# Kernel optimization log

Measured on AMD Instinct MI355X. Metric: run time of the kernel, lower is better.

The kernel has to match this reference:

```python
import jax, jax.numpy as jnp
import numpy as np
from jax import lax

B, C, H, W = 256, 3, 224, 224
M_MAG = 9.0  # RandAugment magnitude (init arg m)


def setup_inputs() -> dict:
    key = jax.random.key(0)
    k1, k2 = jax.random.split(key)
    # CIFAR-style normalization constants (as in the source module)
    mean = jnp.array([0.4914, 0.4822, 0.4465], dtype=jnp.float32)
    std = jnp.array([0.2023, 0.1994, 0.201], dtype=jnp.float32)
    # raw image in [0,1], then normalized (module expects normalized input)
    img = jax.random.uniform(k1, (B, C, H, W), dtype=jnp.float32)
    x = (img - mean[None, :, None, None]) / std[None, :, None, None]
    return {"x": x, "mean": mean, "std": std}


def _forward(x, mean, std):
    # deterministic op chain: sharpness -> contrast -> brightness -> solarize
    v_blend = M_MAG / 30.0 * (1.9 - 0.1) + 0.1   # 0.64 for sharpness/contrast/brightness
    v_sol = M_MAG / 30.0 * 1.0                    # 0.3 solarize threshold
    m_ = mean[None, :, None, None]
    s_ = std[None, :, None, None]

    # denormalize
    y = x * s_ + m_

    # sharpness: blend with 3x3 blur (kernel [[1,1,1],[1,5,1],[1,1,1]]/13, zero pad)
    k = jnp.array([[1., 1., 1.], [1., 5., 1.], [1., 1., 1.]], dtype=y.dtype) / 13.0
    kern = jnp.broadcast_to(k[None, None], (3, 1, 3, 3))  # depthwise OIHW
    blur = lax.conv_general_dilated(
        y, kern, window_strides=(1, 1), padding=[(1, 1), (1, 1)],
        feature_group_count=3, dimension_numbers=("NCHW", "OIHW", "NCHW"))
    y = y * v_blend + blur * (1.0 - v_blend)

    # contrast: blend with per-image mean of grayscale
    gray = 0.299 * y[:, 0] + 0.587 * y[:, 1] + 0.114 * y[:, 2]  # [B,H,W]
    gm = gray.mean(axis=(1, 2))[:, None, None, None]             # [B,1,1,1]
    y = y * v_blend + gm * (1.0 - v_blend)

    # brightness: blend with zeros
    y = y * v_blend

    # solarize: invert pixels >= threshold
    y = jnp.where(y < v_sol, y, 1.0 - y)

    # normalize
    return (y - m_) / s_


def reference(x, mean, std):
    return _forward(x, mean, std)
```

## Files before the change

### kernel.cpp

```cpp
#include <hip/hip_runtime.h>

#define IMG_B 256
#define IMG_H 224
#define IMG_W 224
#define HWPIX 50176
#define YP 228

#define FA(a,b) __fadd_rn((a),(b))
#define FM(a,b) __fmul_rn((a),(b))
#define FS(a,b) __fsub_rn((a),(b))
#define FD(a,b) __fdiv_rn((a),(b))

typedef float nt4 __attribute__((ext_vector_type(4)));

__device__ __forceinline__ float VBF()   { return (float)(9.0/30.0*(1.9-0.1)+0.1); }
__device__ __forceinline__ float OMVBF() { return (float)(1.0 - (9.0/30.0*(1.9-0.1)+0.1)); }
__device__ __forceinline__ float VSF()   { return (float)(9.0/30.0*1.0); }

__device__ __forceinline__ void y1_from_rows(const float* yU, const float* yC,
                                             const float* yD, float* y1o) {
    const float WN = 1.0f / 13.0f, WC = 5.0f / 13.0f;
#pragma unroll
    for (int mm = 0; mm < 4; ++mm) {
        float acc = 0.0f;
        acc = FA(acc, FM(WN, yU[mm + 0]));
        acc = FA(acc, FM(WN, yU[mm + 1]));
        acc = FA(acc, FM(WN, yU[mm + 2]));
        acc = FA(acc, FM(WN, yC[mm + 0]));
        acc = FA(acc, FM(WC, yC[mm + 1]));
        acc = FA(acc, FM(WN, yC[mm + 2]));
        acc = FA(acc, FM(WN, yD[mm + 0]));
        acc = FA(acc, FM(WN, yD[mm + 1]));
        acc = FA(acc, FM(WN, yD[mm + 2]));
        y1o[mm] = FA(FM(yC[mm + 1], VBF()), FM(acc, OMVBF()));
    }
}

__device__ __forceinline__ void stage_load(const float* __restrict__ xc, int r0,
                                           int t, float4* pf) {
#pragma unroll
    for (int u = 0; u < 4; ++u) {
        const int idx = t + 256 * u;
        float4 v = make_float4(0.f, 0.f, 0.f, 0.f);
        if (idx < 896) {
            const int row = idx / 56, c4 = (idx % 56) * 4;
            const int gi = r0 - 1 + row;
            if (gi >= 0 && gi < IMG_H)
                v = *(const float4*)(xc + (size_t)gi * IMG_W + c4);
        }
        pf[u] = v;
    }
}

__device__ __forceinline__ void stage_write(float s, float m, int r0, int t,
                                            const float4* pf, float* __restrict__ Y,
                                            int P) {
#pragma unroll
    for (int u = 0; u < 4; ++u) {
        const int idx = t + 256 * u;
        if (idx < 896) {
            const int row = idx / 56, c4 = (idx % 56) * 4;
            const int gi = r0 - 1 + row;
            float4 w;
            if (gi >= 0 && gi < IMG_H) {
                w.x = FA(FM(pf[u].x, s), m);
                w.y = FA(FM(pf[u].y, s), m);
                w.z = FA(FM(pf[u].z, s), m);
                w.w = FA(FM(pf[u].w, s), m);
            } else {
                w.x = w.y = w.z = w.w = 0.0f;
            }
            *(float4*)(&Y[row * P + c4]) = w;
        }
    }
}

__device__ __forceinline__ void lds_y6(const float* __restrict__ r, int j, float* y6) {
    const float4 vC = *(const float4*)(r + j);
    const float4 vL = *(const float4*)(r + (j > 0 ? j - 4 : 0));
    const float4 vR = *(const float4*)(r + (j + 4 < IMG_W ? j + 4 : IMG_W - 4));
    y6[0] = (j > 0) ? vL.w : 0.0f;
    y6[1] = vC.x; y6[2] = vC.y; y6[3] = vC.z; y6[4] = vC.w;
    y6[5] = (j + 4 < IMG_W) ? vR.x : 0.0f;
}

__global__ __launch_bounds__(256, 4) void kA1(const float* __restrict__ x,
                                              const float* __restrict__ mean_,
                                              const float* __restrict__ std_,
                                              float* __restrict__ part) {
    const int swz = (blockIdx.x & 7) * 512 + (blockIdx.x >> 3);
    const int ck = swz & 15, b = swz >> 4;
    const int t = threadIdx.x;
    const int r0 = ck * 14;

    __shared__ float SM[3648];
    float* Y  = SM;
    float* G2 = SM;
    float* CH = SM + 3328;
    float* LS = SM + 3584;

    const int rg  = t / 56;
    const int col = t - rg * 56;
    const bool active = (t < 224);
    const int rcount = (rg < 2) ? 4 : 3;
    const int rstart = (rg < 2) ? rg * 4 : 8 + (rg - 2) * 3;
    const int jd = col * 4;
    const bool lwave = ((t & 63) == 0)  && (col > 0);
    const bool rwave = ((t & 63) == 63) && (col < 55);

    const float s0 = std_[0], s1 = std_[1], s2 = std_[2];
    const float m0 = mean_[0], m1 = mean_[1], m2 = mean_[2];
    const float C0 = 0.299f, C1 = 0.587f, C2 = 0.114f;

    float4 q0[4], q1[4], q2[4];
#pragma unroll
    for (int u = 0; u < 4; ++u) {
        const int idx = t + 256 * u;
        q0[u] = q1[u] = q2[u] = make_float4(0.f, 0.f, 0.f, 0.f);
        if (idx < 896) {
            const int row = idx / 56, c4 = (idx % 56) * 4;
            const int gi = r0 - 1 + row;
            if (gi >= 0 && gi < IMG_H) {
                const float* p = x + (size_t)b * 3 * HWPIX + (size_t)gi * IMG_W + c4;
                q0[u] = *(const float4*)(p);
                q1[u] = *(const float4*)(p + HWPIX);
                q2[u] = *(const float4*)(p + 2 * HWPIX);
            }
        }
    }
#define GRAY1(a0v, a1v, a2v)                                              \
    FA(FA(FM(C0, FA(FM(a0v, s0), m0)), FM(C1, FA(FM(a1v, s1), m1))),      \
       FM(C2, FA(FM(a2v, s2), m2)))
#pragma unroll
    for (int u = 0; u < 4; ++u) {
        const int idx = t + 256 * u;
        if (idx < 896) {
            const int row = idx / 56, c4 = (idx % 56) * 4;
            const int gi = r0 - 1 + row;
            float4 w = make_float4(0.f, 0.f, 0.f, 0.f);
            if (gi >= 0 && gi < IMG_H) {
                w.x = GRAY1(q0[u].x, q1[u].x, q2[u].x);
                w.y = GRAY1(q0[u].y, q1[u].y, q2[u].y);
                w.z = GRAY1(q0[u].z, q1[u].z, q2[u].z);
                w.w = GRAY1(q0[u].w, q1[u].w, q2[u].w);
            }
            *(float4*)(&Y[row * YP + c4]) = w;
        }
    }
#undef GRAY1
    __syncthreads();

#define LOADROW(V, LWv, RWv, yr) do {                                 \
        V   = *(const float4*)(&Y[(yr) * YP + jd]);                   \
        LWv = __shfl_up(V.w, 1, 64);                                  \
        RWv = __shfl_down(V.x, 1, 64);                                \
        if (lwave) LWv = Y[(yr) * YP + jd - 1];                       \
        if (rwave) RWv = Y[(yr) * YP + jd + 4];                       \
    } while (0)

#define FILL6(y6, V, LWv, RWv) do {                                   \
        y6[0] = (col > 0) ? LWv : 0.0f;                               \
        y6[1] = V.x; y6[2] = V.y; y6[3] = V.z; y6[4] = V.w;           \
        y6[5] = (col < 55) ? RWv : 0.0f;                              \
    } while (0)

    float4 gacc[4];

    if (active) {
        float4 v0, v1, v2;
        float la0, la1, la2, ra0, ra1, ra2;
        LOADROW(v0, la0, ra0, rstart);
        LOADROW(v1, la1, ra1, rstart + 1);
#pragma unroll
        for (int k = 0; k < 4; ++k) {
            if (k < rcount) {
                LOADROW(v2, la2, ra2, rstart + k + 2);
                float yU[6], yC[6], yD[6], y1g[4];
                FILL6(yU, v0, la0, ra0);
                FILL6(yC, v1, la1, ra1);
                FILL6(yD, v2, la2, ra2);
                y1_from_rows(yU, yC, yD, y1g);
                gacc[k].x = y1g[0]; gacc[k].y = y1g[1];
                gacc[k].z = y1g[2]; gacc[k].w = y1g[3];
                v0 = v1; la0 = la1; ra0 = ra1;
                v1 = v2; la1 = la2; ra1 = ra2;
            }
        }
    }
    __syncthreads();

    if (active) {
#pragma unroll
        for (int k = 0; k < 4; ++k) {
            if (k < rcount) {
                const int pl = (rstart + k) * IMG_W + jd;
                const int grp = pl / 392;
                const int rem = pl - grp * 392;
                int li = rem / 96; if (li > 3) li = 3;
                const int o = rem - 96 * li;
                *(float4*)(&G2[(grp * 4 + li) * 104 + o]) = gacc[k];
            }
        }
    }
    __syncthreads();

    {
        const int leaf = t >> 3, e = t & 7;
        const int base = leaf * 104 + e;
        const int nk = ((leaf & 3) == 3) ? 13 : 12;
        float r = G2[base];
        for (int k = 1; k < nk; ++k) r = FA(r, G2[base + 8 * k]);
        CH[t] = r;
    }
    __syncthreads();

    if (t < 32) {
        const float* c8 = &CH[t * 8];
        LS[t] = FA(FA(FA(c8[0], c8[1]), FA(c8[2], c8[3])),
                   FA(FA(c8[4], c8[5]), FA(c8[6], c8[7])));
    }
    __syncthreads();

    if (t == 0) {
        float v[32];
#pragma unroll
        for (int k = 0; k < 32; ++k) v[k] = LS[k];
        for (int n = 16; n >= 1; n >>= 1)
            for (int k = 0; k < n; ++k) v[k] = FA(v[2 * k], v[2 * k + 1]);
        part[swz] = v[0];
    }
#undef LOADROW
#undef FILL6
}

__global__ __launch_bounds__(256) void kB(const float* __restrict__ x,
                                          const float* __restrict__ mean_,
                                          const float* __restrict__ std_,
                                          const float* __restrict__ part,
                                          float* __restrict__ out) {
    const int swz = ((int)blockIdx.x & 7) * 1536 + ((int)blockIdx.x >> 3);
    const int ck = swz & 15;
    const int r1 = swz >> 4;
    const int c  = r1 % 3;
    const int b  = r1 / 3;
    const int t  = threadIdx.x;
    const int r0 = ck * 14;

    __shared__ float Y[16 * IMG_W];
    __shared__ float gsh;

    const float s = std_[c], m = mean_[c];
    float4 pf[4];
    stage_load(x + (size_t)(b * 3 + c) * HWPIX, r0, t, pf);

    if (t == 0) {
        float v[16];
#pragma unroll
        for (int k = 0; k < 16; ++k) v[k] = part[b * 16 + k];
#pragma unroll
        for (int n = 8; n >= 1; n >>= 1)
#pragma unroll
            for (int k = 0; k < 8; ++k)
                if (k < n) v[k] = FA(v[2 * k], v[2 * k + 1]);
        gsh = FD(v[0], 50176.0f);
    }

    stage_write(s, m, r0, t, pf, Y, IMG_W);
    __syncthreads();
    const float g = gsh;

    float* oc = out + (size_t)(b * 3 + c) * HWPIX + (size_t)r0 * IMG_W;

    for (int qi = t; qi < 784; qi += 256) {
        const int lr = qi / 56 + 1, j = (qi % 56) * 4;
        float yU[6], yC[6], yD[6], y1[4];
        lds_y6(&Y[(lr - 1) * IMG_W], j, yU);
        lds_y6(&Y[lr * IMG_W],       j, yC);
        lds_y6(&Y[(lr + 1) * IMG_W], j, yD);
        y1_from_rows(yU, yC, yD, y1);

        nt4 o4;
#pragma unroll
        for (int mm = 0; mm < 4; ++mm) {
            const float y2 = FA(FM(y1[mm], VBF()), FM(g, OMVBF()));
            const float y3 = FM(y2, VBF());
            const float y4 = (y3 < VSF()) ? y3 : FS(1.0f, y3);
            o4[mm] = FD(FS(y4, m), s);
        }
        __builtin_nontemporal_store(o4, (nt4*)(oc + (size_t)(lr - 1) * IMG_W + j));
    }
}

extern "C" void kernel_launch(void* const* d_in, const int* in_sizes, int n_in,
                              void* d_out, int out_size, void* d_ws, size_t ws_size,
                              hipStream_t stream) {
    const float* x     = (const float*)d_in[0];
    const float* mean_ = (const float*)d_in[1];
    const float* std_  = (const float*)d_in[2];
    float* out = (float*)d_out;

    float* part = (float*)d_ws;

    kA1<<<IMG_B * 16, 256, 0, stream>>>(x, mean_, std_, part);

    kB<<<IMG_B * 3 * 16, 256, 0, stream>>>(x, mean_, std_, part, out);
}
```

Before: 77.04 us.

## Load raw tile directly to LDS and denormalize on read; shuffle-reduce partials

kB now copies the raw input halo tile from global memory straight into LDS with global_load_lds, instead of staging through registers and writing denormalized values. The denormalize affine is applied when values are read back from LDS, and out-of-range halo rows are clamped on load and zeroed on read. This removes the register round-trip and the separate LDS write pass, at the cost of redoing the multiply-add on each of the repeated stencil reads. In kA1, the last 32-way reduction is done with wave shuffles, which drops one LDS buffer, one barrier and the serial single-thread sum.

```diff
diff --git a/kernel.cpp b/kernel.cpp
--- a/kernel.cpp
+++ b/kernel.cpp
@@ -1,4 +1,5 @@
 #include <hip/hip_runtime.h>
+#include <stdint.h>
 
 #define IMG_B 256
 #define IMG_H 224
@@ -36,52 +37,22 @@
     }
 }
 
-__device__ __forceinline__ void stage_load(const float* __restrict__ xc, int r0,
-                                           int t, float4* pf) {
-#pragma unroll
-    for (int u = 0; u < 4; ++u) {
-        const int idx = t + 256 * u;
-        float4 v = make_float4(0.f, 0.f, 0.f, 0.f);
-        if (idx < 896) {
-            const int row = idx / 56, c4 = (idx % 56) * 4;
-            const int gi = r0 - 1 + row;
-            if (gi >= 0 && gi < IMG_H)
-                v = *(const float4*)(xc + (size_t)gi * IMG_W + c4);
-        }
-        pf[u] = v;
-    }
-}
-
-__device__ __forceinline__ void stage_write(float s, float m, int r0, int t,
-                                            const float4* pf, float* __restrict__ Y,
-                                            int P) {
-#pragma unroll
-    for (int u = 0; u < 4; ++u) {
-        const int idx = t + 256 * u;
-        if (idx < 896) {
-            const int row = idx / 56, c4 = (idx % 56) * 4;
-            const int gi = r0 - 1 + row;
-            float4 w;
-            if (gi >= 0 && gi < IMG_H) {
-                w.x = FA(FM(pf[u].x, s), m);
-                w.y = FA(FM(pf[u].y, s), m);
-                w.z = FA(FM(pf[u].z, s), m);
-                w.w = FA(FM(pf[u].w, s), m);
-            } else {
-                w.x = w.y = w.z = w.w = 0.0f;
-            }
-            *(float4*)(&Y[row * P + c4]) = w;
-        }
-    }
-}
-
-__device__ __forceinline__ void lds_y6(const float* __restrict__ r, int j, float* y6) {
+__device__ __forceinline__ void ldsx_y6(const float* __restrict__ r, int j,
+                                        bool rowvalid, float s, float m, float* y6) {
+    if (!rowvalid) {
+#pragma unroll
+        for (int q = 0; q < 6; ++q) y6[q] = 0.0f;
+        return;
+    }
     const float4 vC = *(const float4*)(r + j);
     const float4 vL = *(const float4*)(r + (j > 0 ? j - 4 : 0));
     const float4 vR = *(const float4*)(r + (j + 4 < IMG_W ? j + 4 : IMG_W - 4));
-    y6[0] = (j > 0) ? vL.w : 0.0f;
-    y6[1] = vC.x; y6[2] = vC.y; y6[3] = vC.z; y6[4] = vC.w;
-    y6[5] = (j + 4 < IMG_W) ? vR.x : 0.0f;
+    y6[0] = (j > 0) ? FA(FM(vL.w, s), m) : 0.0f;
+    y6[1] = FA(FM(vC.x, s), m);
+    y6[2] = FA(FM(vC.y, s), m);
+    y6[3] = FA(FM(vC.z, s), m);
+    y6[4] = FA(FM(vC.w, s), m);
+    y6[5] = (j + 4 < IMG_W) ? FA(FM(vR.x, s), m) : 0.0f;
 }
 
 __global__ __launch_bounds__(256, 4) void kA1(const float* __restrict__ x,
@@ -97,7 +68,6 @@
     float* Y  = SM;
     float* G2 = SM;
     float* CH = SM + 3328;
-    float* LS = SM + 3584;
 
     const int rg  = t / 56;
     const int col = t - rg * 56;
@@ -216,18 +186,15 @@
 
     if (t < 32) {
         const float* c8 = &CH[t * 8];
-        LS[t] = FA(FA(FA(c8[0], c8[1]), FA(c8[2], c8[3])),
-                   FA(FA(c8[4], c8[5]), FA(c8[6], c8[7])));
-    }
-    __syncthreads();
-
-    if (t == 0) {
-        float v[32];
-#pragma unroll
-        for (int k = 0; k < 32; ++k) v[k] = LS[k];
-        for (int n = 16; n >= 1; n >>= 1)
-            for (int k = 0; k < n; ++k) v[k] = FA(v[2 * k], v[2 * k + 1]);
-        part[swz] = v[0];
+        float vv = FA(FA(FA(c8[0], c8[1]), FA(c8[2], c8[3])),
+                      FA(FA(c8[4], c8[5]), FA(c8[6], c8[7])));
+#pragma unroll
+        for (int n = 16; n >= 1; n >>= 1) {
+            const float lo = __shfl(vv, 2 * t, 64);
+            const float hi = __shfl(vv, 2 * t + 1, 64);
+            vv = FA(lo, hi);
+        }
+        if (t == 0) part[swz] = vv;
     }
 #undef LOADROW
 #undef FILL6
@@ -246,12 +213,25 @@
     const int t  = threadIdx.x;
     const int r0 = ck * 14;
 
-    __shared__ float Y[16 * IMG_W];
+    __shared__ float X[16 * IMG_W];
     __shared__ float gsh;
 
     const float s = std_[c], m = mean_[c];
-    float4 pf[4];
-    stage_load(x + (size_t)(b * 3 + c) * HWPIX, r0, t, pf);
+    const float* xc = x + (size_t)(b * 3 + c) * HWPIX;
+
+#pragma unroll
+    for (int u = 0; u < 4; ++u) {
+        const int idx = t + 256 * u;
+        if (idx < 896) {
+            int gi = r0 - 1 + idx / 56;
+            gi = gi < 0 ? 0 : (gi > IMG_H - 1 ? IMG_H - 1 : gi);
+            const float* src = xc + (size_t)gi * IMG_W + (idx % 56) * 4;
+            __builtin_amdgcn_global_load_lds(
+                (const __attribute__((address_space(1))) uint32_t*)src,
+                (__attribute__((address_space(3))) uint32_t*)(&X[(size_t)idx * 4]),
+                16, 0, 0);
+        }
+    }
 
     if (t == 0) {
         float v[16];
@@ -264,8 +244,6 @@
                 if (k < n) v[k] = FA(v[2 * k], v[2 * k + 1]);
         gsh = FD(v[0], 50176.0f);
     }
-
-    stage_write(s, m, r0, t, pf, Y, IMG_W);
     __syncthreads();
     const float g = gsh;
 
@@ -273,10 +251,11 @@
 
     for (int qi = t; qi < 784; qi += 256) {
         const int lr = qi / 56 + 1, j = (qi % 56) * 4;
+        const int gU = r0 + lr - 2, gD = r0 + lr;
         float yU[6], yC[6], yD[6], y1[4];
-        lds_y6(&Y[(lr - 1) * IMG_W], j, yU);
-        lds_y6(&Y[lr * IMG_W],       j, yC);
-        lds_y6(&Y[(lr + 1) * IMG_W], j, yD);
+        ldsx_y6(&X[(lr - 1) * IMG_W], j, (gU >= 0),     s, m, yU);
+        ldsx_y6(&X[lr * IMG_W],       j, true,          s, m, yC);
+        ldsx_y6(&X[(lr + 1) * IMG_W], j, (gD < IMG_H),  s, m, yD);
         y1_from_rows(yU, yC, yD, y1);
 
         nt4 o4;
```

Measured after the change: 82.69 us. 1.07x slower.
